# Performance work log

Hardware: AMD Instinct MI355X
Metric: run time of the kernel (lower is better)

The kernel has to match this reference:

```python
import math
import jax, jax.numpy as jnp
import numpy as np

N_HEADS = 16
THETA = 10000.0


def _rope_cos_sin(S, head_dim):
    half = head_dim // 2
    inv_freq = 1.0 / (THETA ** (jnp.arange(half, dtype=jnp.float32) / half))
    t = jnp.arange(S, dtype=jnp.float32)
    freqs = t[:, None] * inv_freq[None, :]  # [S, half]
    return jnp.cos(freqs), jnp.sin(freqs)


def _apply_rope(x, cos, sin):
    # x: [B, H, S, D] float32; cos/sin: [S, D//2]
    half = x.shape[-1] // 2
    x1, x2 = x[..., :half], x[..., half:]
    c = cos[None, None, :, :]
    s = sin[None, None, :, :]
    return jnp.concatenate([x1 * c - x2 * s, x1 * s + x2 * c], axis=-1)


def setup_inputs() -> dict:
    key = jax.random.key(0)
    k1, k2, k3 = jax.random.split(key, 3)
    B, S, D = 4, 2048, 1024
    x = jax.random.normal(k1, (B, S, D), dtype=jnp.float32)
    w_qkv = jax.random.normal(k2, (3 * D, D), dtype=jnp.float32) * (1.0 / math.sqrt(D))
    w_out = jax.random.normal(k3, (D, D), dtype=jnp.float32) * (1.0 / math.sqrt(D))
    return {"x": x, "w_qkv": w_qkv, "w_out": w_out}


def reference(x, w_qkv, w_out):
    B, S, D = x.shape
    H = N_HEADS
    hd = D // H

    qkv = x @ w_qkv.T  # [B, S, 3D]
    q, k, v = jnp.split(qkv, 3, axis=-1)

    def reshape(t):
        return t.reshape(B, S, H, hd).transpose(0, 2, 1, 3)  # [B,H,S,hd]

    q, k, v = reshape(q), reshape(k), reshape(v)

    cos, sin = _rope_cos_sin(S, hd)
    q = _apply_rope(q.astype(jnp.float32), cos, sin).astype(x.dtype)
    k = _apply_rope(k.astype(jnp.float32), cos, sin).astype(x.dtype)

    scale = math.sqrt(hd)
    scores = jnp.einsum("bhsd,bhtd->bhst", q, k) / scale  # [B,H,S,S]
    causal = jnp.tril(jnp.ones((S, S), dtype=bool))
    scores = jnp.where(causal[None, None], scores, -jnp.inf)
    attn = jax.nn.softmax(scores.astype(jnp.float32), axis=-1).astype(x.dtype)

    out = jnp.einsum("bhst,bhtd->bhsd", attn, v)  # [B,H,S,hd]
    out = out.transpose(0, 2, 1, 3).reshape(B, S, D)
    return out @ w_out.T
```

## Files before the change

### kernel.cpp

```cpp
#include <hip/hip_runtime.h>
#include <hip/hip_bf16.h>

#define DEV static __device__ __forceinline__

typedef unsigned short u16;
typedef unsigned int u32;
typedef __attribute__((ext_vector_type(8))) short short8;
typedef __attribute__((ext_vector_type(4))) float f32x4;
typedef __attribute__((ext_vector_type(16))) float f32x16;
typedef __attribute__((ext_vector_type(4))) u32 u32x4;

static constexpr int Bsz = 4, Ssz = 2048, Dsz = 1024, Hn = 16, HD = 64;
static constexpr int Mrows = Bsz * Ssz;

DEV u16 f2bu(float f) {
  union { float f; u32 u; } a; a.f = f;
  u32 u = a.u;
  u32 r = (u + 0x7FFFu + ((u >> 16) & 1u)) >> 16;
  return (u16)r;
}
DEV float b2f(u16 v) {
  union { u32 u; float f; } a; a.u = ((u32)v) << 16;
  return a.f;
}
DEV u32 pk2(float lo, float hi2) {
  __hip_bfloat162 t = __float22bfloat162_rn(make_float2(lo, hi2));
  u32 r; __builtin_memcpy(&r, &t, 4); return r;
}
DEV f32x16 mfma3232(short8 a, short8 b, f32x16 c) {
  return __builtin_amdgcn_mfma_f32_32x32x16_bf16(a, b, c, 0, 0, 0);
}
DEV float ex2(float x) { return __builtin_amdgcn_exp2f(x); }

__global__ void k_cast(const float4* __restrict__ in, ushort4* __restrict__ out, int n4) {
  int stride = gridDim.x * blockDim.x;
  for (int i = blockIdx.x * blockDim.x + threadIdx.x; i < n4; i += stride) {
    float4 v = in[i];
    ushort4 o;
    o.x = f2bu(v.x); o.y = f2bu(v.y); o.z = f2bu(v.z); o.w = f2bu(v.w);
    out[i] = o;
  }
}

__global__ void k_ropetab(float2* __restrict__ cst) {
  int i = blockIdx.x * blockDim.x + threadIdx.x;
  if (i >= Ssz * 32) return;
  int s = i >> 5, d = i & 31;
  float inv = powf(10000.0f, -(float)d / 32.0f);
  float fr = (float)s * inv;
  cst[i] = make_float2(cosf(fr), sinf(fr));
}

DEV void cp16(const u16* g, u16* l) {
  __builtin_amdgcn_global_load_lds((const __attribute__((address_space(1))) u32*)g,
                                   (__attribute__((address_space(3))) u32*)l, 16, 0, 0);
}

template <bool OUTBF16>
__global__ __launch_bounds__(256, 2) void k_gemm(const u16* __restrict__ A,
                                                 const u16* __restrict__ W,
                                                 void* __restrict__ C, int N, int K,
                                                 const float2* __restrict__ cst, int cpx,
                                                 u16* __restrict__ vtp) {
  __shared__ __align__(16) u16 SMEM[33792];
  const int tid = threadIdx.x;
  const int wid = tid >> 6, lane = tid & 63;
  const int lr = lane & 15, u = lane >> 4;
  const int wm = wid >> 1, wn = wid & 1;

  const int wg = blockIdx.x;
  const int xcd = wg & 7;
  const int j = wg >> 3;
  const int brow = (j / cpx) * 128;
  const int bcol = (xcd * cpx + j % cpx) * 128;

  const int rw = wid * 32 + (lane >> 3);
  const int octS = ((lane & 7) ^ (rw & 7)) * 8;
  const u16* aS = A + (size_t)(brow + rw) * K + octS;
  const u16* bS = W + (size_t)(bcol + rw) * K + octS;
  const int dBase = wid * 2048 + lane * 8;

  const int aBase = (wm * 64 + lr) * 64;
  const int bBase = (wn * 64 + lr) * 64;
  const int o0 = (u ^ (lane & 7)) * 8;
  const int o1 = ((4 + u) ^ (lane & 7)) * 8;

  f32x4 acc[4][4];
#pragma unroll
  for (int i = 0; i < 4; ++i)
#pragma unroll
    for (int j2 = 0; j2 < 4; ++j2) acc[i][j2] = (f32x4){0.f, 0.f, 0.f, 0.f};

  const int nt = K >> 6;

#define STG(kk, bb)                                                    \
  do {                                                                 \
    u16* ad = SMEM + (bb)*8192 + dBase;                                \
    u16* bd = SMEM + 16384 + (bb)*8192 + dBase;                        \
    cp16(aS + (kk), ad);                                               \
    cp16(aS + (size_t)8 * K + (kk), ad + 512);                         \
    cp16(aS + (size_t)16 * K + (kk), ad + 1024);                       \
    cp16(aS + (size_t)24 * K + (kk), ad + 1536);                       \
    cp16(bS + (kk), bd);                                               \
    cp16(bS + (size_t)8 * K + (kk), bd + 512);                         \
    cp16(bS + (size_t)16 * K + (kk), bd + 1024);                       \
    cp16(bS + (size_t)24 * K + (kk), bd + 1536);                       \
  } while (0)

  STG(0, 0);

  for (int t = 0; t < nt; ++t) {
    asm volatile("s_waitcnt vmcnt(0)" ::: "memory");
    __builtin_amdgcn_s_barrier();
    if (t + 1 < nt) STG((t + 1) << 6, (t + 1) & 1);
    const u16* ab = SMEM + (t & 1) * 8192;
    const u16* bb = SMEM + 16384 + (t & 1) * 8192;
    short8 a0[4], a1[4], b0[4], b1[4];
#pragma unroll
    for (int mr = 0; mr < 4; ++mr) {
      a0[mr] = *(const short8*)(ab + aBase + mr * 1024 + o0);
      a1[mr] = *(const short8*)(ab + aBase + mr * 1024 + o1);
    }
#pragma unroll
    for (int nr = 0; nr < 4; ++nr) {
      b0[nr] = *(const short8*)(bb + bBase + nr * 1024 + o0);
      b1[nr] = *(const short8*)(bb + bBase + nr * 1024 + o1);
    }
    __builtin_amdgcn_s_setprio(1);
#pragma unroll
    for (int mr = 0; mr < 4; ++mr)
#pragma unroll
      for (int nr = 0; nr < 4; ++nr)
        acc[mr][nr] =
            __builtin_amdgcn_mfma_f32_16x16x32_bf16(a0[mr], b0[nr], acc[mr][nr], 0, 0, 0);
#pragma unroll
    for (int mr = 0; mr < 4; ++mr)
#pragma unroll
      for (int nr = 0; nr < 4; ++nr)
        acc[mr][nr] =
            __builtin_amdgcn_mfma_f32_16x16x32_bf16(a1[mr], b1[nr], acc[mr][nr], 0, 0, 0);
    __builtin_amdgcn_s_setprio(0);
  }
#undef STG

  if (OUTBF16) {
    __syncthreads();
    const int rmode = (bcol < 1024) ? 0 : (bcol < 2048) ? 1 : 2;
    if (rmode < 2) {
      const float sc = (rmode == 0) ? 0.18033688f : 1.0f;
#pragma unroll
      for (int mr = 0; mr < 4; ++mr)
#pragma unroll
        for (int r = 0; r < 4; ++r) {
          const int row = wm * 64 + mr * 16 + u * 4 + r;
          const int s = (brow + row) & 2047;
          const float2 c0 = cst[s * 32 + lr];
          const float2 c1 = cst[s * 32 + 16 + lr];
          const float x10 = acc[mr][0][r], x11 = acc[mr][1][r];
          const float x20 = acc[mr][2][r], x21 = acc[mr][3][r];
          u16* lp = SMEM + row * 136 + wn * 64 + lr;
          lp[0]  = f2bu((x10 * c0.x - x20 * c0.y) * sc);
          lp[16] = f2bu((x11 * c1.x - x21 * c1.y) * sc);
          lp[32] = f2bu((x10 * c0.y + x20 * c0.x) * sc);
          lp[48] = f2bu((x11 * c1.y + x21 * c1.x) * sc);
        }
      __syncthreads();
      u16* cp = (u16*)C;
#pragma unroll
      for (int i = 0; i < 8; ++i) {
        const int e = i * 2048 + tid * 8;
        const int row = e >> 7, col = e & 127;
        short8 v = *(const short8*)(SMEM + row * 136 + col);
        *(short8*)(cp + (size_t)(brow + row) * N + bcol + col) = v;
      }
    } else {
#pragma unroll
      for (int mr = 0; mr < 4; ++mr)
#pragma unroll
        for (int nr = 0; nr < 4; ++nr)
#pragma unroll
          for (int r = 0; r < 4; ++r) {
            const int dl = wn * 64 + nr * 16 + lr;
            const int sl = wm * 64 + mr * 16 + u * 4 + r;
            SMEM[dl * 136 + sl] = f2bu(acc[mr][nr][r]);
          }
      __syncthreads();
      const int bb2 = brow >> 11;
      const int sbase = brow & 2047;
#pragma unroll
      for (int i = 0; i < 8; ++i) {
        const int e = i * 2048 + tid * 8;
        const int dl = e >> 7, sl = e & 127;
        const int gd = (bcol - 2048) + dl;
        short8 v = *(const short8*)(SMEM + dl * 136 + sl);
        *(short8*)(vtp + (size_t)(bb2 * 1024 + gd) * 2048 + sbase + sl) = v;
      }
    }
  } else {
    __syncthreads();
    float* FS = (float*)SMEM;
#pragma unroll
    for (int mr = 0; mr < 4; ++mr)
#pragma unroll
      for (int nr = 0; nr < 4; ++nr)
#pragma unroll
        for (int r = 0; r < 4; ++r)
          FS[(wm * 64 + mr * 16 + u * 4 + r) * 132 + wn * 64 + nr * 16 + lr] =
              acc[mr][nr][r];
    __syncthreads();
    float* cp = (float*)C;
#pragma unroll
    for (int i = 0; i < 16; ++i) {
      const int e = i * 1024 + tid * 4;
      const int row = e >> 7, col = e & 127;
      float4 v = *(const float4*)(FS + row * 132 + col);
      *(float4*)(cp + (size_t)(brow + row) * N + bcol + col) = v;
    }
  }
}

__global__ __launch_bounds__(256, 4) void k_attn(const u16* __restrict__ qkv,
                                                 const u16* __restrict__ vt,
                                                 u16* __restrict__ obuf) {
  __shared__ __align__(16) u16 Ksm[2][64 * 64];
  __shared__ __align__(16) u16 Vsm[2][64 * 64];

  const int tid = threadIdx.x;
  const int wid = tid >> 6;
  const int lane = tid & 63;
  const int l31 = lane & 31;
  const int hi = lane >> 5;
  const int r7 = l31 & 7;

  const int fid = blockIdx.x;
  const int a = fid & 3, bq = (fid >> 8) & 3;
  const int bh = (fid >> 2) & 63;
  const int sel = a ^ bq;
  const int qt = (sel == 0) ? bq : (sel == 1) ? 7 - bq : (sel == 2) ? 8 + bq : 15 - bq;

  const int b = bh >> 4;
  const int h = bh & 15;

  const float NEG = -__builtin_inff();

  const int srow = lane >> 3;
  const int scol = ((lane & 7) ^ srow) * 8;
  const u16* ksrc0 = qkv + (size_t)(b * Ssz + wid * 16 + srow) * 3072 + 1024 + h * 64 + scol;
  const u16* ksrc1 = ksrc0 + (size_t)8 * 3072;
  const u16* vsrc0 = vt + ((size_t)bh * 64 + wid * 16 + srow) * Ssz + scol;
  const u16* vsrc1 = vsrc0 + (size_t)8 * Ssz;
  u16* kD0 = Ksm[0] + wid * 1024;
  u16* vD0 = Vsm[0] + wid * 1024;

  const int q0 = qt * 128;
  const int qrow = q0 + (wid << 5) + l31;

  const u16* qptr = qkv + (size_t)(b * Ssz + qrow) * 3072 + h * 64 + hi * 8;
  short8 qf[4];
#pragma unroll
  for (int s = 0; s < 4; ++s) qf[s] = *(const short8*)(qptr + s * 16);

  f32x16 o0 = {0.f}, o1 = {0.f};
  float lsum = 0.f;

  const int ntiles = 2 * qt + 2;
  const int lastT = 2 * qt + (wid >> 1);

  cp16(ksrc0, kD0);
  cp16(ksrc1, kD0 + 512);
  cp16(vsrc0, vD0);
  cp16(vsrc1, vD0 + 512);

  const u16* kS0 = ksrc0 + (size_t)64 * 3072;
  const u16* kS1 = ksrc1 + (size_t)64 * 3072;
  const u16* vS0 = vsrc0 + 64;
  const u16* vS1 = vsrc1 + 64;

  for (int t = 0; t < ntiles; ++t) {
    __syncthreads();
    if (t + 1 < ntiles) {
      const int nb = (t + 1) & 1;
      cp16(kS0, kD0 + nb * 4096);
      cp16(kS1, kD0 + nb * 4096 + 512);
      cp16(vS0, vD0 + nb * 4096);
      cp16(vS1, vD0 + nb * 4096 + 512);
      kS0 += (size_t)64 * 3072;
      kS1 += (size_t)64 * 3072;
      vS0 += 64;
      vS1 += 64;
    }
    if (t > lastT) continue;

    const u16* kbuf = Ksm[t & 1];
    const u16* vbuf = Vsm[t & 1];
    const int kv0 = t << 6;

    f32x16 st0 = {0.f}, st1 = {0.f};
    __builtin_amdgcn_s_setprio(1);
#pragma unroll
    for (int s = 0; s < 4; ++s) {
      const int slot = (((2 * s + hi) ^ r7) << 3);
      short8 k0 = *(const short8*)(kbuf + l31 * 64 + slot);
      short8 k1 = *(const short8*)(kbuf + (32 + l31) * 64 + slot);
      st0 = mfma3232(k0, qf[s], st0);
      st1 = mfma3232(k1, qf[s], st1);
    }
    __builtin_amdgcn_s_setprio(0);

    if (t == lastT) {
      const int kb0 = kv0 + 4 * hi;
#pragma unroll
      for (int r = 0; r < 16; ++r) {
        const int ko = (r & 3) + 8 * (r >> 2);
        if (kb0 + ko > qrow) st0[r] = NEG;
        if (kb0 + 32 + ko > qrow) st1[r] = NEG;
      }
    }

    float rsp[4] = {0.f, 0.f, 0.f, 0.f};
#pragma unroll
    for (int r = 0; r < 16; ++r) {
      const float p0 = ex2(st0[r]);
      const float p1 = ex2(st1[r]);
      st0[r] = p0;
      st1[r] = p1;
      rsp[r & 3] += p0 + p1;
    }
    float rs = (rsp[0] + rsp[1]) + (rsp[2] + rsp[3]);
    rs += __shfl_xor(rs, 32);
    lsum += rs;

    u32 wa[8], wb[8];
#pragma unroll
    for (int g = 0; g < 4; ++g) {
      wa[g] = pk2(st0[4 * g + 0], st0[4 * g + 1]);
      wb[g] = pk2(st0[4 * g + 2], st0[4 * g + 3]);
      wa[4 + g] = pk2(st1[4 * g + 0], st1[4 * g + 1]);
      wb[4 + g] = pk2(st1[4 * g + 2], st1[4 * g + 3]);
    }

#pragma unroll
    for (int s = 0; s < 4; ++s) {
      const u32 uA0 = wa[2 * s], uA1 = wa[2 * s + 1];
      const u32 uB0 = wb[2 * s], uB1 = wb[2 * s + 1];
      const u32 tA0 = __shfl_xor(uA0, 32), tA1 = __shfl_xor(uA1, 32);
      const u32 tB0 = __shfl_xor(uB0, 32), tB1 = __shfl_xor(uB1, 32);
      u32x4 pw;
      pw.x = hi ? tA1 : uA0;
      pw.y = hi ? tB1 : uB0;
      pw.z = hi ? uA1 : tA0;
      pw.w = hi ? uB1 : tB0;
      short8 pfrag = *(short8*)&pw;
      const int slot = (((2 * s + hi) ^ r7) << 3);
      short8 v0 = *(const short8*)(vbuf + l31 * 64 + slot);
      short8 v1 = *(const short8*)(vbuf + (32 + l31) * 64 + slot);
      __builtin_amdgcn_s_setprio(1);
      o0 = mfma3232(v0, pfrag, o0);
      o1 = mfma3232(v1, pfrag, o1);
      __builtin_amdgcn_s_setprio(0);
    }
  }

  const float inv = 1.0f / lsum;
  u16* orow = obuf + (size_t)(b * Ssz + qrow) * 1024 + h * 64;
#pragma unroll
  for (int j = 0; j < 4; ++j) {
    ushort4 s0, s1;
    s0.x = f2bu(o0[4 * j + 0] * inv);
    s0.y = f2bu(o0[4 * j + 1] * inv);
    s0.z = f2bu(o0[4 * j + 2] * inv);
    s0.w = f2bu(o0[4 * j + 3] * inv);
    s1.x = f2bu(o1[4 * j + 0] * inv);
    s1.y = f2bu(o1[4 * j + 1] * inv);
    s1.z = f2bu(o1[4 * j + 2] * inv);
    s1.w = f2bu(o1[4 * j + 3] * inv);
    *(ushort4*)(orow + 8 * j + 4 * hi) = s0;
    *(ushort4*)(orow + 32 + 8 * j + 4 * hi) = s1;
  }
}

extern "C" void kernel_launch(void* const* d_in, const int* in_sizes, int n_in,
                              void* d_out, int out_size, void* d_ws, size_t ws_size,
                              hipStream_t stream) {
  const float* x = (const float*)d_in[0];
  const float* wqkv = (const float*)d_in[1];
  const float* wout = (const float*)d_in[2];

  char* ws = (char*)d_ws;
  u16* xb      = (u16*)(ws + 0);
  u16* wqkvb   = (u16*)(ws + 16777216);
  u16* woutb   = (u16*)(ws + 23068672);
  u16* qkv     = (u16*)(ws + 25165824);
  u16* vt      = (u16*)(ws + 75497472);
  u16* obuf    = (u16*)(ws + 92274688);
  float2* cst  = (float2*)(ws + 109051904);

  k_cast<<<2048, 256, 0, stream>>>((const float4*)x, (ushort4*)xb, Mrows * Dsz / 4);
  k_cast<<<2048, 256, 0, stream>>>((const float4*)wqkv, (ushort4*)wqkvb, 3 * Dsz * Dsz / 4);
  k_cast<<<1024, 256, 0, stream>>>((const float4*)wout, (ushort4*)woutb, Dsz * Dsz / 4);
  k_ropetab<<<256, 256, 0, stream>>>(cst);

  k_gemm<true><<<1536, 256, 0, stream>>>(xb, wqkvb, qkv, 3072, 1024, cst, 3, vt);

  k_attn<<<1024, 256, 0, stream>>>(qkv, vt, obuf);

  k_gemm<false><<<512, 256, 0, stream>>>(obuf, woutb, d_out, 1024, 1024, nullptr, 1, nullptr);
}
```

Baseline: 173.8 us.

## Split attention KV tile across two wave groups and fuse cast kernels

The attention kernel now runs 512 threads per block. Each pair of waves splits the 64-key tile into two 32-key halves, so each wave does half the QK and PV MFMAs per tile. The partial outputs and row sums are then merged through shared memory at the end. This gives more waves per block to hide latency and finer causal skipping, at the cost of extra syncs and an LDS reduction. The three fp32-to-bf16 cast launches are also merged into a single kernel to cut launch overhead.

```diff
diff --git a/kernel.cpp b/kernel.cpp
--- a/kernel.cpp
+++ b/kernel.cpp
@@ -32,13 +32,20 @@
 }
 DEV float ex2(float x) { return __builtin_amdgcn_exp2f(x); }
 
-__global__ void k_cast(const float4* __restrict__ in, ushort4* __restrict__ out, int n4) {
-  int stride = gridDim.x * blockDim.x;
-  for (int i = blockIdx.x * blockDim.x + threadIdx.x; i < n4; i += stride) {
-    float4 v = in[i];
+__global__ void k_cast3(const float4* __restrict__ s0, ushort4* __restrict__ d0, int n0,
+                        const float4* __restrict__ s1, ushort4* __restrict__ d1, int n1,
+                        const float4* __restrict__ s2, ushort4* __restrict__ d2, int n2) {
+  const int stride = gridDim.x * blockDim.x;
+  const int total = n0 + n1 + n2;
+  for (int i = blockIdx.x * blockDim.x + threadIdx.x; i < total; i += stride) {
+    const float4* s; ushort4* d; int k;
+    if (i < n0) { s = s0; d = d0; k = i; }
+    else if (i < n0 + n1) { s = s1; d = d1; k = i - n0; }
+    else { s = s2; d = d2; k = i - n0 - n1; }
+    float4 v = s[k];
     ushort4 o;
     o.x = f2bu(v.x); o.y = f2bu(v.y); o.z = f2bu(v.z); o.w = f2bu(v.w);
-    out[i] = o;
+    d[k] = o;
   }
 }
 
@@ -219,11 +226,10 @@
   }
 }
 
-__global__ __launch_bounds__(256, 4) void k_attn(const u16* __restrict__ qkv,
+__global__ __launch_bounds__(512, 6) void k_attn(const u16* __restrict__ qkv,
                                                  const u16* __restrict__ vt,
                                                  u16* __restrict__ obuf) {
-  __shared__ __align__(16) u16 Ksm[2][64 * 64];
-  __shared__ __align__(16) u16 Vsm[2][64 * 64];
+  __shared__ __align__(16) u16 SM[16384];
 
   const int tid = threadIdx.x;
   const int wid = tid >> 6;
@@ -232,6 +238,9 @@
   const int hi = lane >> 5;
   const int r7 = l31 & 7;
 
+  const int m = wid >> 2;
+  const int s4 = wid & 3;
+
   const int fid = blockIdx.x;
   const int a = fid & 3, bq = (fid >> 8) & 3;
   const int bh = (fid >> 2) & 63;
@@ -245,15 +254,11 @@
 
   const int srow = lane >> 3;
   const int scol = ((lane & 7) ^ srow) * 8;
-  const u16* ksrc0 = qkv + (size_t)(b * Ssz + wid * 16 + srow) * 3072 + 1024 + h * 64 + scol;
-  const u16* ksrc1 = ksrc0 + (size_t)8 * 3072;
-  const u16* vsrc0 = vt + ((size_t)bh * 64 + wid * 16 + srow) * Ssz + scol;
-  const u16* vsrc1 = vsrc0 + (size_t)8 * Ssz;
-  u16* kD0 = Ksm[0] + wid * 1024;
-  u16* vD0 = Vsm[0] + wid * 1024;
+  const u16* kS = qkv + (size_t)(b * Ssz + wid * 8 + srow) * 3072 + 1024 + h * 64 + scol;
+  const u16* vS = vt + ((size_t)bh * 64 + wid * 8 + srow) * Ssz + scol;
 
   const int q0 = qt * 128;
-  const int qrow = q0 + (wid << 5) + l31;
+  const int qrow = q0 + (s4 << 5) + l31;
 
   const u16* qptr = qkv + (size_t)(b * Ssz + qrow) * 3072 + h * 64 + hi * 8;
   short8 qf[4];
@@ -264,85 +269,67 @@
   float lsum = 0.f;
 
   const int ntiles = 2 * qt + 2;
-  const int lastT = 2 * qt + (wid >> 1);
-
-  cp16(ksrc0, kD0);
-  cp16(ksrc1, kD0 + 512);
-  cp16(vsrc0, vD0);
-  cp16(vsrc1, vD0 + 512);
-
-  const u16* kS0 = ksrc0 + (size_t)64 * 3072;
-  const u16* kS1 = ksrc1 + (size_t)64 * 3072;
-  const u16* vS0 = vsrc0 + 64;
-  const u16* vS1 = vsrc1 + 64;
+  const int lastT = (q0 + (s4 << 5) + 31 - 32 * m) >> 6;
+
+  cp16(kS, SM + wid * 512);
+  cp16(vS, SM + 8192 + wid * 512);
+  const u16* kSp = kS + (size_t)64 * 3072;
+  const u16* vSp = vS + 64;
 
   for (int t = 0; t < ntiles; ++t) {
     __syncthreads();
     if (t + 1 < ntiles) {
       const int nb = (t + 1) & 1;
-      cp16(kS0, kD0 + nb * 4096);
-      cp16(kS1, kD0 + nb * 4096 + 512);
-      cp16(vS0, vD0 + nb * 4096);
-      cp16(vS1, vD0 + nb * 4096 + 512);
-      kS0 += (size_t)64 * 3072;
-      kS1 += (size_t)64 * 3072;
-      vS0 += 64;
-      vS1 += 64;
+      cp16(kSp, SM + nb * 4096 + wid * 512);
+      cp16(vSp, SM + 8192 + nb * 4096 + wid * 512);
+      kSp += (size_t)64 * 3072;
+      vSp += 64;
     }
     if (t > lastT) continue;
 
-    const u16* kbuf = Ksm[t & 1];
-    const u16* vbuf = Vsm[t & 1];
+    const u16* kbuf = SM + (t & 1) * 4096;
+    const u16* vbuf = SM + 8192 + (t & 1) * 4096;
     const int kv0 = t << 6;
 
-    f32x16 st0 = {0.f}, st1 = {0.f};
+    f32x16 st = {0.f};
     __builtin_amdgcn_s_setprio(1);
 #pragma unroll
     for (int s = 0; s < 4; ++s) {
       const int slot = (((2 * s + hi) ^ r7) << 3);
-      short8 k0 = *(const short8*)(kbuf + l31 * 64 + slot);
-      short8 k1 = *(const short8*)(kbuf + (32 + l31) * 64 + slot);
-      st0 = mfma3232(k0, qf[s], st0);
-      st1 = mfma3232(k1, qf[s], st1);
+      short8 k0 = *(const short8*)(kbuf + (32 * m + l31) * 64 + slot);
+      st = mfma3232(k0, qf[s], st);
     }
     __builtin_amdgcn_s_setprio(0);
 
     if (t == lastT) {
-      const int kb0 = kv0 + 4 * hi;
+      const int kb0 = kv0 + 32 * m + 4 * hi;
 #pragma unroll
       for (int r = 0; r < 16; ++r) {
-        const int ko = (r & 3) + 8 * (r >> 2);
-        if (kb0 + ko > qrow) st0[r] = NEG;
-        if (kb0 + 32 + ko > qrow) st1[r] = NEG;
+        if (kb0 + (r & 3) + 8 * (r >> 2) > qrow) st[r] = NEG;
       }
     }
 
     float rsp[4] = {0.f, 0.f, 0.f, 0.f};
 #pragma unroll
     for (int r = 0; r < 16; ++r) {
-      const float p0 = ex2(st0[r]);
-      const float p1 = ex2(st1[r]);
-      st0[r] = p0;
-      st1[r] = p1;
-      rsp[r & 3] += p0 + p1;
-    }
-    float rs = (rsp[0] + rsp[1]) + (rsp[2] + rsp[3]);
-    rs += __shfl_xor(rs, 32);
-    lsum += rs;
-
-    u32 wa[8], wb[8];
+      const float p = ex2(st[r]);
+      st[r] = p;
+      rsp[r & 3] += p;
+    }
+    lsum += (rsp[0] + rsp[1]) + (rsp[2] + rsp[3]);
+
+    u32 wa[4], wb[4];
 #pragma unroll
     for (int g = 0; g < 4; ++g) {
-      wa[g] = pk2(st0[4 * g + 0], st0[4 * g + 1]);
-      wb[g] = pk2(st0[4 * g + 2], st0[4 * g + 3]);
-      wa[4 + g] = pk2(st1[4 * g + 0], st1[4 * g + 1]);
-      wb[4 + g] = pk2(st1[4 * g + 2], st1[4 * g + 3]);
-    }
-
-#pragma unroll
-    for (int s = 0; s < 4; ++s) {
-      const u32 uA0 = wa[2 * s], uA1 = wa[2 * s + 1];
-      const u32 uB0 = wb[2 * s], uB1 = wb[2 * s + 1];
+      wa[g] = pk2(st[4 * g + 0], st[4 * g + 1]);
+      wb[g] = pk2(st[4 * g + 2], st[4 * g + 3]);
+    }
+
+#pragma unroll
+    for (int jj = 0; jj < 2; ++jj) {
+      const int s = 2 * m + jj;
+      const u32 uA0 = wa[2 * jj], uA1 = wa[2 * jj + 1];
+      const u32 uB0 = wb[2 * jj], uB1 = wb[2 * jj + 1];
       const u32 tA0 = __shfl_xor(uA0, 32), tA1 = __shfl_xor(uA1, 32);
       const u32 tB0 = __shfl_xor(uB0, 32), tB1 = __shfl_xor(uB1, 32);
       u32x4 pw;
@@ -361,21 +348,47 @@
     }
   }
 
-  const float inv = 1.0f / lsum;
-  u16* orow = obuf + (size_t)(b * Ssz + qrow) * 1024 + h * 64;
-#pragma unroll
-  for (int j = 0; j < 4; ++j) {
-    ushort4 s0, s1;
-    s0.x = f2bu(o0[4 * j + 0] * inv);
-    s0.y = f2bu(o0[4 * j + 1] * inv);
-    s0.z = f2bu(o0[4 * j + 2] * inv);
-    s0.w = f2bu(o0[4 * j + 3] * inv);
-    s1.x = f2bu(o1[4 * j + 0] * inv);
-    s1.y = f2bu(o1[4 * j + 1] * inv);
-    s1.z = f2bu(o1[4 * j + 2] * inv);
-    s1.w = f2bu(o1[4 * j + 3] * inv);
-    *(ushort4*)(orow + 8 * j + 4 * hi) = s0;
-    *(ushort4*)(orow + 32 + 8 * j + 4 * hi) = s1;
+  float* MG = (float*)SM;
+  __syncthreads();
+  if (m == 1) {
+    MG[s4 * 64 + lane] = lsum;
+#pragma unroll
+    for (int j = 0; j < 16; ++j) MG[256 + j * 256 + s4 * 64 + lane] = o0[j];
+  }
+  __syncthreads();
+  if (m == 0) {
+    lsum += MG[s4 * 64 + lane];
+#pragma unroll
+    for (int j = 0; j < 16; ++j) o0[j] += MG[256 + j * 256 + s4 * 64 + lane];
+  }
+  __syncthreads();
+  if (m == 1) {
+#pragma unroll
+    for (int j = 0; j < 16; ++j) MG[256 + j * 256 + s4 * 64 + lane] = o1[j];
+  }
+  __syncthreads();
+  if (m == 0) {
+#pragma unroll
+    for (int j = 0; j < 16; ++j) o1[j] += MG[256 + j * 256 + s4 * 64 + lane];
+
+    const float lt = lsum + __shfl_xor(lsum, 32);
+    const float inv = 1.0f / lt;
+
+    u16* orow = obuf + (size_t)(b * Ssz + qrow) * 1024 + h * 64;
+#pragma unroll
+    for (int j = 0; j < 4; ++j) {
+      ushort4 s0, s1;
+      s0.x = f2bu(o0[4 * j + 0] * inv);
+      s0.y = f2bu(o0[4 * j + 1] * inv);
+      s0.z = f2bu(o0[4 * j + 2] * inv);
+      s0.w = f2bu(o0[4 * j + 3] * inv);
+      s1.x = f2bu(o1[4 * j + 0] * inv);
+      s1.y = f2bu(o1[4 * j + 1] * inv);
+      s1.z = f2bu(o1[4 * j + 2] * inv);
+      s1.w = f2bu(o1[4 * j + 3] * inv);
+      *(ushort4*)(orow + 8 * j + 4 * hi) = s0;
+      *(ushort4*)(orow + 32 + 8 * j + 4 * hi) = s1;
+    }
   }
 }
 
@@ -395,14 +408,15 @@
   u16* obuf    = (u16*)(ws + 92274688);
   float2* cst  = (float2*)(ws + 109051904);
 
-  k_cast<<<2048, 256, 0, stream>>>((const float4*)x, (ushort4*)xb, Mrows * Dsz / 4);
-  k_cast<<<2048, 256, 0, stream>>>((const float4*)wqkv, (ushort4*)wqkvb, 3 * Dsz * Dsz / 4);
-  k_cast<<<1024, 256, 0, stream>>>((const float4*)wout, (ushort4*)woutb, Dsz * Dsz / 4);
+  k_cast3<<<2048, 256, 0, stream>>>(
+      (const float4*)x, (ushort4*)xb, Mrows * Dsz / 4,
+      (const float4*)wqkv, (ushort4*)wqkvb, 3 * Dsz * Dsz / 4,
+      (const float4*)wout, (ushort4*)woutb, Dsz * Dsz / 4);
   k_ropetab<<<256, 256, 0, stream>>>(cst);
 
   k_gemm<true><<<1536, 256, 0, stream>>>(xb, wqkvb, qkv, 3072, 1024, cst, 3, vt);
 
-  k_attn<<<1024, 256, 0, stream>>>(qkv, vt, obuf);
+  k_attn<<<1024, 512, 0, stream>>>(qkv, vt, obuf);
 
   k_gemm<false><<<512, 256, 0, stream>>>(obuf, woutb, d_out, 1024, 1024, nullptr, 1, nullptr);
 }
```

Result: slower. 199.5 us (+14.8%).
